# Performance work log

Measured on AMD Instinct MI355X. Metric: run time of the kernel, lower is better.

## Reference

```python
import jax, jax.numpy as jnp
import numpy as np

LN_EPS = 1e-5
CLAMP = 1e-8


def _linear(x, W, b):
    return x @ W + b


def _layernorm(x, g, b):
    mu = x.mean(-1, keepdims=True)
    var = ((x - mu) ** 2).mean(-1, keepdims=True)
    return (x - mu) / jnp.sqrt(var + LN_EPS) * g + b


def _residual(x, W1, b1, W2, b2):
    return jax.nn.relu(_linear(jax.nn.relu(_linear(x, W1, b1)), W2, b2)) + x


def _forward(node_emb, attn_Wq, attn_bq, attn_Wk, attn_bk, attn_Wv, attn_bv,
             attn_Wd, attn_bd, attn_ln_g, attn_ln_b,
             mlp_r1_w1, mlp_r1_b1, mlp_r1_w2, mlp_r1_b2,
             mlp_r2_w1, mlp_r2_b1, mlp_r2_w2, mlp_r2_b2,
             mlp_out_w, mlp_out_b,
             log_phi_r0, log_phi_r1h, log_phi_r1v, log_phi_r2, r0_idx, n):
    x = node_emb  # [1, n^2, D]
    L = attn_Wq.shape[0]
    for l in range(L):  # mask in the original is all zeros -> plain softmax attention
        q = _linear(x, attn_Wq[l], attn_bq[l])
        k = _linear(x, attn_Wk[l], attn_bk[l])
        v = _linear(x, attn_Wv[l], attn_bv[l])
        probs = jax.nn.softmax(jnp.einsum('bqd,bkd->bqk', q, k), axis=-1)
        ctx = jnp.einsum('bqk,bkd->bqd', probs, v)
        x = _layernorm(_linear(ctx, attn_Wd[l], attn_bd[l]) + x, attn_ln_g[l], attn_ln_b[l])
    x0 = x[0]                                  # [n^2, D]
    feats = x0[r0_idx].reshape(r0_idx.shape[0], -1)  # [R0, 4D]
    h = _residual(feats, mlp_r1_w1, mlp_r1_b1, mlp_r1_w2, mlp_r1_b2)
    h = _residual(h, mlp_r2_w1, mlp_r2_b1, mlp_r2_w2, mlp_r2_b2)
    logits = _linear(h, mlp_out_w, mlp_out_b)  # [R0, 16]
    beliefs = jax.nn.softmax(logits, axis=-1).reshape(-1, 2, 2, 2, 2)

    m = n - 1  # plaquettes per row
    # --- R1 horizontal interior edges (row r in 1..n-2, col c in 0..n-2) ---
    r, c = np.meshgrid(np.arange(1, n - 1), np.arange(m), indexing='ij')
    above = ((r - 1) * m + c).ravel()
    below = (r * m + c).ravel()
    h_stack = jnp.stack([beliefs[above].sum((1, 2)),   # edge nodes at plaquette pos 2,3
                         beliefs[below].sum((3, 4))])  # edge nodes at plaquette pos 0,1
    h_bel = h_stack.mean(0)                            # [Eh,2,2]
    mism = jnp.sum((h_stack - h_bel) ** 2)
    # --- R1 vertical interior edges (row r in 0..n-2, col c in 1..n-2) ---
    r, c = np.meshgrid(np.arange(m), np.arange(1, n - 1), indexing='ij')
    left = (r * m + (c - 1)).ravel()
    right = (r * m + c).ravel()
    v_stack = jnp.stack([beliefs[left].sum((1, 3)),    # edge nodes at pos 1,3
                         beliefs[right].sum((2, 4))])  # edge nodes at pos 0,2
    v_bel = v_stack.mean(0)                            # [Ev,2,2]
    mism = mism + jnp.sum((v_stack - v_bel) ** 2)
    # --- R2 interior nodes (r, c in 1..n-2), parents are the 4 incident edges ---
    r, c = np.meshgrid(np.arange(1, n - 1), np.arange(1, n - 1), indexing='ij')
    hl = ((r - 1) * m + (c - 1)).ravel()
    hr = ((r - 1) * m + c).ravel()
    vu = ((r - 1) * (n - 2) + (c - 1)).ravel()
    vd = (r * (n - 2) + (c - 1)).ravel()
    n_stack = jnp.stack([h_bel[hl].sum(1), h_bel[hr].sum(2),
                         v_bel[vu].sum(1), v_bel[vd].sum(2)])
    n_bel = n_stack.mean(0)                            # [V,2]
    mism = mism + jnp.sum((n_stack - n_bel) ** 2)

    # --- Kikuchi energy: counts +1 (plaquette), -1 (edge), +1 (node); log_phi detached ---
    def reg_energy(b, lphi, cnt):
        bc = jnp.maximum(b, CLAMP)
        return cnt * jnp.sum(bc * (jnp.log(bc) - jax.lax.stop_gradient(lphi)))

    energy = (reg_energy(beliefs, log_phi_r0, 1.0)
              + reg_energy(h_bel, log_phi_r1h, -1.0)
              + reg_energy(v_bel, log_phi_r1v, -1.0)
              + reg_energy(n_bel, log_phi_r2, 1.0))
    return energy, mism


def setup_inputs() -> dict:
    n, D, L, HID, OUT = 64, 256, 2, 1024, 16
    m = n - 1
    R0, E, V = m * m, (n - 2) * m, (n - 2) * (n - 2)
    key = jax.random.key(0)
    ks = jax.random.split(key, 24)
    norm = lambda k, sh, s=0.05: jax.random.normal(k, sh, dtype=jnp.float32) * s
    r, c = np.meshgrid(np.arange(m), np.arange(m), indexing='ij')
    i = (r * n + c).ravel()
    r0_idx = jnp.asarray(np.stack([i, i + 1, i + n, i + n + 1], 1), dtype=jnp.int32)
    inp = {
        'node_emb': jax.random.normal(ks[0], (1, n * n, D), dtype=jnp.float32),
        'attn_Wq': norm(ks[1], (L, D, D)), 'attn_bq': jnp.zeros((L, D), jnp.float32),
        'attn_Wk': norm(ks[2], (L, D, D)), 'attn_bk': jnp.zeros((L, D), jnp.float32),
        'attn_Wv': norm(ks[3], (L, D, D)), 'attn_bv': jnp.zeros((L, D), jnp.float32),
        'attn_Wd': norm(ks[4], (L, D, D)), 'attn_bd': jnp.zeros((L, D), jnp.float32),
        'attn_ln_g': jnp.ones((L, D), jnp.float32), 'attn_ln_b': jnp.zeros((L, D), jnp.float32),
        'mlp_r1_w1': norm(ks[5], (HID, HID), 0.03), 'mlp_r1_b1': jnp.zeros((HID,), jnp.float32),
        'mlp_r1_w2': norm(ks[6], (HID, HID), 0.03), 'mlp_r1_b2': jnp.zeros((HID,), jnp.float32),
        'mlp_r2_w1': norm(ks[7], (HID, HID), 0.03), 'mlp_r2_b1': jnp.zeros((HID,), jnp.float32),
        'mlp_r2_w2': norm(ks[8], (HID, HID), 0.03), 'mlp_r2_b2': jnp.zeros((HID,), jnp.float32),
        'mlp_out_w': norm(ks[9], (HID, OUT), 0.03), 'mlp_out_b': jnp.zeros((OUT,), jnp.float32),
        'log_phi_r0': jax.random.normal(ks[10], (R0, 2, 2, 2, 2), dtype=jnp.float32),
        'log_phi_r1h': jax.random.normal(ks[11], (E, 2, 2), dtype=jnp.float32),
        'log_phi_r1v': jax.random.normal(ks[12], (E, 2, 2), dtype=jnp.float32),
        'log_phi_r2': jax.random.normal(ks[13], (V, 2), dtype=jnp.float32),
        'r0_idx': r0_idx,
        'n': n,
    }
    return inp


def reference(node_emb, attn_Wq, attn_bq, attn_Wk, attn_bk, attn_Wv, attn_bv,
              attn_Wd, attn_bd, attn_ln_g, attn_ln_b,
              mlp_r1_w1, mlp_r1_b1, mlp_r1_w2, mlp_r1_b2,
              mlp_r2_w1, mlp_r2_b1, mlp_r2_w2, mlp_r2_b2,
              mlp_out_w, mlp_out_b,
              log_phi_r0, log_phi_r1h, log_phi_r1v, log_phi_r2, r0_idx, n):
    return _forward(node_emb, attn_Wq, attn_bq, attn_Wk, attn_bk, attn_Wv, attn_bv,
                    attn_Wd, attn_bd, attn_ln_g, attn_ln_b,
                    mlp_r1_w1, mlp_r1_b1, mlp_r1_w2, mlp_r1_b2,
                    mlp_r2_w1, mlp_r2_b1, mlp_r2_w2, mlp_r2_b2,
                    mlp_out_w, mlp_out_b,
                    log_phi_r0, log_phi_r1h, log_phi_r1v, log_phi_r2, r0_idx, n)
```

## Files before the change

kernel.cpp:

```cpp
#include <hip/hip_runtime.h>
#include <hip/hip_bf16.h>
#include <math.h>

#define D_    256
#define NSQ   4096
#define NL    2
#define HID_  1024
#define R0_   3969
#define EH_   3906
#define EV_   3906
#define NV_   3844
#define LN_EPS_ 1e-5f
#define CLAMP_  1e-8f
#define TK_    64

typedef float f32x4 __attribute__((ext_vector_type(4)));
typedef __bf16 bf16x8 __attribute__((ext_vector_type(8)));
typedef unsigned short u16x8 __attribute__((ext_vector_type(8)));

__device__ __forceinline__ void gload_lds16(const void* g, void* l) {
    __builtin_amdgcn_global_load_lds(
        (const __attribute__((address_space(1))) void*)g,
        (__attribute__((address_space(3))) void*)l, 16, 0, 0);
}

template<int BM, int BN>
__device__ __forceinline__ void gemm_body(
    const __hip_bfloat16* __restrict__ A, const __hip_bfloat16* __restrict__ Bt,
    const float* __restrict__ bias,
    const float* __restrict__ resf, const __hip_bfloat16* __restrict__ resb,
    void* __restrict__ C, int M, int N, int K, int relu, int outmode,
    int bx, int by)
{
    constexpr int WR  = BM / 64;
    constexpr int WC  = 4 / WR;
    constexpr int WNT = BN / WC;
    constexpr int NF  = WNT / 16;
    constexpr int ACH = BM / 64;
    constexpr int BCH = BN / 64;
    constexpr int ASZ = BM * 32;

    __shared__ __hip_bfloat16 sm[2][(BM + BN) * 32];

    const int t = threadIdx.x;
    const int lane = t & 63, wave = t >> 6;
    const int ln = lane & 15, lg = lane >> 4;
    const int wr = (WR == 1) ? 0 : (wave >> 1);
    const int wc = (WR == 1) ? wave : (wave & 1);
    const int row0 = bx * BM, col0 = by * BN;

    int aoff[ACH], boff[BCH];
    #pragma unroll
    for (int c = 0; c < ACH; ++c) {
        int e = (c * 256 + t) * 8;
        int row = e >> 5, slot = (e >> 3) & 3;
        int kg = slot ^ (row & 3) ^ ((row >> 2) & 3);
        aoff[c] = row * K + kg * 8;
    }
    #pragma unroll
    for (int c = 0; c < BCH; ++c) {
        int e = (c * 256 + t) * 8;
        int row = e >> 5, slot = (e >> 3) & 3;
        int kg = slot ^ (row & 3) ^ ((row >> 2) & 3);
        boff[c] = row * K + kg * 8;
    }
    const int sw = (ln & 3) ^ ((ln >> 2) & 3);

    const __hip_bfloat16* Ab = A + (size_t)row0 * K;
    const __hip_bfloat16* Bb = Bt + (size_t)col0 * K;

    f32x4 acc[4][NF];
    #pragma unroll
    for (int m = 0; m < 4; ++m)
        #pragma unroll
        for (int n = 0; n < NF; ++n) acc[m][n] = f32x4{0.f, 0.f, 0.f, 0.f};

    auto STAGE = [&](int k0, int buf) {
        #pragma unroll
        for (int c = 0; c < ACH; ++c)
            gload_lds16(Ab + k0 + aoff[c], (char*)&sm[buf][0] + (c * 256 + t) * 16);
        #pragma unroll
        for (int c = 0; c < BCH; ++c)
            gload_lds16(Bb + k0 + boff[c], (char*)&sm[buf][ASZ] + (c * 256 + t) * 16);
    };

    STAGE(0, 0);
    __syncthreads();
    int cur = 0;
    for (int k0 = 0; k0 < K; k0 += 32) {
        if (k0 + 32 < K) STAGE(k0 + 32, cur ^ 1);
        bf16x8 af[4], bfr[NF];
        #pragma unroll
        for (int m = 0; m < 4; ++m)
            af[m] = *(const bf16x8*)((const char*)&sm[cur][0] +
                     (size_t)(wr * 64 + m * 16 + ln) * 64 + ((lg ^ sw) << 4));
        #pragma unroll
        for (int n = 0; n < NF; ++n)
            bfr[n] = *(const bf16x8*)((const char*)&sm[cur][ASZ] +
                     (size_t)(wc * WNT + n * 16 + ln) * 64 + ((lg ^ sw) << 4));
        #pragma unroll
        for (int m = 0; m < 4; ++m)
            #pragma unroll
            for (int n = 0; n < NF; ++n)
                acc[m][n] = __builtin_amdgcn_mfma_f32_16x16x32_bf16(
                    af[m], bfr[n], acc[m][n], 0, 0, 0);
        __syncthreads();
        cur ^= 1;
    }

    #pragma unroll
    for (int m = 0; m < 4; ++m) {
        const int rowb = row0 + wr * 64 + m * 16 + lg * 4;
        #pragma unroll
        for (int n = 0; n < NF; ++n) {
            const int col = col0 + wc * WNT + n * 16 + ln;
            const float bv = bias ? bias[col] : 0.f;
            if (outmode == 2) {
                union { ushort4 u4; __hip_bfloat16 h[4]; } pk;
                #pragma unroll
                for (int r = 0; r < 4; ++r) {
                    float v = acc[m][n][r] + bv;
                    if (relu) v = fmaxf(v, 0.f);
                    pk.h[r] = __float2bfloat16(v);
                }
                *(ushort4*)((__hip_bfloat16*)C + (size_t)col * M + rowb) = pk.u4;
            } else if (outmode == 3) {
                union { ushort4 u4; __hip_bfloat16 h[4]; } pk;
                #pragma unroll
                for (int r = 0; r < 4; ++r) {
                    float v = acc[m][n][r] + bv;
                    if (relu) v = fmaxf(v, 0.f);
                    pk.h[r] = __float2bfloat16(v);
                }
                size_t off = ((size_t)((rowb >> 5) * 16 + (col >> 4)) << 9)
                           + (size_t)(((rowb >> 3) & 3) * 16 + (col & 15)) * 8
                           + (rowb & 7);
                *(ushort4*)((__hip_bfloat16*)C + off) = pk.u4;
            } else {
                #pragma unroll
                for (int r = 0; r < 4; ++r) {
                    float v = acc[m][n][r] + bv;
                    if (relu) v = fmaxf(v, 0.f);
                    const size_t idx = (size_t)(rowb + r) * N + col;
                    if (resf) v += resf[idx];
                    if (resb) v += __bfloat162float(resb[idx]);
                    if (outmode == 0) ((float*)C)[idx] = v;
                    else ((__hip_bfloat16*)C)[idx] = __float2bfloat16(v);
                }
            }
        }
    }
}

template<int BM, int BN>
__global__ __launch_bounds__(256) void gemm_t(
    const __hip_bfloat16* __restrict__ A, const __hip_bfloat16* __restrict__ Bt,
    const float* __restrict__ bias,
    const float* __restrict__ resf, const __hip_bfloat16* __restrict__ resb,
    void* __restrict__ C, int M, int N, int K, int relu, int outmode)
{
    gemm_body<BM, BN>(A, Bt, bias, resf, resb, C, M, N, K, relu, outmode,
                      blockIdx.x, blockIdx.y);
}

__global__ __launch_bounds__(256) void gemm_qkv(
    const __hip_bfloat16* __restrict__ xb,
    const __hip_bfloat16* __restrict__ wqkt2, const __hip_bfloat16* __restrict__ wvt2,
    const float* __restrict__ bqk2, const float* __restrict__ bv,
    __hip_bfloat16* __restrict__ qkb, __hip_bfloat16* __restrict__ vf, int l)
{
    const __hip_bfloat16* Bt;
    const float* bias;
    void* C;
    int N, outmode, by;
    if (blockIdx.y < 4) {
        Bt = wqkt2 + (size_t)l * 131072; bias = bqk2 + l * 512;
        C = qkb; N = 512; outmode = 1; by = blockIdx.y;
    } else {
        Bt = wvt2 + (size_t)l * 65536; bias = bv + l * D_;
        C = vf; N = D_; outmode = 3; by = blockIdx.y - 4;
    }
    gemm_body<64, 128>(xb, Bt, bias, nullptr, nullptr, C, NSQ, N, D_, 0, outmode,
                       blockIdx.x, by);
}

__global__ __launch_bounds__(512, 4) void gemm_128(
    const __hip_bfloat16* __restrict__ A, const __hip_bfloat16* __restrict__ Bt,
    const float* __restrict__ bias, const __hip_bfloat16* __restrict__ resb,
    __hip_bfloat16* __restrict__ C, int M, int N, int K, int relu)
{
    __shared__ __hip_bfloat16 sm[2][8192];

    const int t = threadIdx.x;
    const int lane = t & 63, wave = t >> 6;
    const int ln = lane & 15, lg = lane >> 4;
    const int wr = wave >> 2, wc = wave & 3;
    const int row0 = blockIdx.x * 128, col0 = blockIdx.y * 128;

    const int srow = t >> 2, sslot = t & 3;
    const int skg = sslot ^ (srow & 3) ^ ((srow >> 2) & 3);
    const int soff = srow * K + skg * 8;
    const int sw = (ln & 3) ^ ((ln >> 2) & 3);

    const __hip_bfloat16* Ab = A + (size_t)row0 * K;
    const __hip_bfloat16* Bb = Bt + (size_t)col0 * K;

    f32x4 acc[4][2];
    #pragma unroll
    for (int m = 0; m < 4; ++m)
        #pragma unroll
        for (int n = 0; n < 2; ++n) acc[m][n] = f32x4{0.f, 0.f, 0.f, 0.f};

    auto STAGE = [&](int k0, int buf) {
        gload_lds16(Ab + k0 + soff, (char*)&sm[buf][0] + t * 16);
        gload_lds16(Bb + k0 + soff, (char*)&sm[buf][4096] + t * 16);
    };

    STAGE(0, 0);
    __syncthreads();
    int cur = 0;
    for (int k0 = 0; k0 < K; k0 += 32) {
        if (k0 + 32 < K) STAGE(k0 + 32, cur ^ 1);
        bf16x8 af[4], bfr[2];
        #pragma unroll
        for (int m = 0; m < 4; ++m)
            af[m] = *(const bf16x8*)((const char*)&sm[cur][0] +
                     (size_t)(wr * 64 + m * 16 + ln) * 64 + ((lg ^ sw) << 4));
        #pragma unroll
        for (int n = 0; n < 2; ++n)
            bfr[n] = *(const bf16x8*)((const char*)&sm[cur][4096] +
                     (size_t)(wc * 32 + n * 16 + ln) * 64 + ((lg ^ sw) << 4));
        #pragma unroll
        for (int m = 0; m < 4; ++m)
            #pragma unroll
            for (int n = 0; n < 2; ++n)
                acc[m][n] = __builtin_amdgcn_mfma_f32_16x16x32_bf16(
                    af[m], bfr[n], acc[m][n], 0, 0, 0);
        __syncthreads();
        cur ^= 1;
    }

    #pragma unroll
    for (int m = 0; m < 4; ++m) {
        const int rowb = row0 + wr * 64 + m * 16 + lg * 4;
        #pragma unroll
        for (int n = 0; n < 2; ++n) {
            const int col = col0 + wc * 32 + n * 16 + ln;
            const float bv = bias[col];
            #pragma unroll
            for (int r = 0; r < 4; ++r) {
                float v = acc[m][n][r] + bv;
                if (relu) v = fmaxf(v, 0.f);
                const size_t idx = (size_t)(rowb + r) * N + col;
                if (resb) v += __bfloat162float(resb[idx]);
                C[idx] = __float2bfloat16(v);
            }
        }
    }
}

__global__ __launch_bounds__(256) void gemm_n16b(
    const __hip_bfloat16* __restrict__ A, const __hip_bfloat16* __restrict__ Bt,
    const float* __restrict__ bias, const float* __restrict__ lphi0,
    float* __restrict__ beliefs, float* __restrict__ out, int M, int K)
{
    const int t = threadIdx.x, lane = t & 63, wave = t >> 6;
    const int ln = lane & 15, lg = lane >> 4;
    const int r0 = blockIdx.x * 64 + wave * 16;
    f32x4 acc = {0.f, 0.f, 0.f, 0.f};
    for (int k0 = 0; k0 < K; k0 += 32) {
        bf16x8 a = *(const bf16x8*)(A + (size_t)(r0 + ln) * K + k0 + lg * 8);
        bf16x8 b = *(const bf16x8*)(Bt + (size_t)ln * K + k0 + lg * 8);
        acc = __builtin_amdgcn_mfma_f32_16x16x32_bf16(a, b, acc, 0, 0, 0);
    }
    float e = 0.f;
    #pragma unroll
    for (int r = 0; r < 4; ++r) {
        const int row = r0 + lg * 4 + r;
        float v = acc[r] + bias[ln];
        float mx = v;
        mx = fmaxf(mx, __shfl_xor(mx, 1));
        mx = fmaxf(mx, __shfl_xor(mx, 2));
        mx = fmaxf(mx, __shfl_xor(mx, 4));
        mx = fmaxf(mx, __shfl_xor(mx, 8));
        float ex = __expf(v - mx);
        float s = ex;
        s += __shfl_xor(s, 1);
        s += __shfl_xor(s, 2);
        s += __shfl_xor(s, 4);
        s += __shfl_xor(s, 8);
        if (row < R0_) {
            float bb = ex / s;
            beliefs[(size_t)row * 16 + ln] = bb;
            float bc = fmaxf(bb, CLAMP_);
            e += bc * (logf(bc) - lphi0[(size_t)row * 16 + ln]);
        }
    }
    #pragma unroll
    for (int off = 32; off; off >>= 1) e += __shfl_down(e, off);
    if (lane == 0) atomicAdd(&out[0], e);
}

__global__ __launch_bounds__(256) void prep_k(
    const float* __restrict__ node_emb, __hip_bfloat16* __restrict__ xb,
    const float* __restrict__ outw, __hip_bfloat16* __restrict__ outwt,
    const float* __restrict__ Wq, const float* __restrict__ Wk,
    const float* __restrict__ Wv, const float* __restrict__ Wd,
    __hip_bfloat16* __restrict__ wqkt2, __hip_bfloat16* __restrict__ wvt2,
    __hip_bfloat16* __restrict__ wdt2,
    const float* __restrict__ bq, const float* __restrict__ bk,
    float* __restrict__ bqk2,
    const float* __restrict__ M0, const float* __restrict__ M1,
    const float* __restrict__ M2, const float* __restrict__ M3,
    __hip_bfloat16* __restrict__ T0, __hip_bfloat16* __restrict__ T1,
    __hip_bfloat16* __restrict__ T2, __hip_bfloat16* __restrict__ T3)
{
    __shared__ float tile[32][33];
    const int b = blockIdx.x, t = threadIdx.x;
    if (b < 1024) {
        int p = b * 256 + t;
        float4 v = *(const float4*)(node_emb + (size_t)p * 4);
        union { ushort4 u4; __hip_bfloat16 h[4]; } pk;
        pk.h[0] = __float2bfloat16(v.x); pk.h[1] = __float2bfloat16(v.y);
        pk.h[2] = __float2bfloat16(v.z); pk.h[3] = __float2bfloat16(v.w);
        *(ushort4*)(xb + (size_t)p * 4) = pk.u4;
    } else if (b < 1088) {
        int i = (b - 1024) * 256 + t;
        int n = i >> 10, k = i & 1023;
        outwt[i] = __float2bfloat16(outw[k * 16 + n]);
    } else if (b < 1600) {
        int idx = b - 1088;
        int z = idx >> 6, bx = (idx >> 3) & 7, by = idx & 7;
        int l = z >> 2, w = z & 3;
        const float* W = (w == 0 ? Wq : w == 1 ? Wk : w == 2 ? Wv : Wd) + (size_t)l * 65536;
        __hip_bfloat16* Wt = w == 0 ? wqkt2 + (size_t)l * 131072
                           : w == 1 ? wqkt2 + (size_t)l * 131072 + 65536
                           : w == 2 ? wvt2 + (size_t)l * 65536
                                    : wdt2 + (size_t)l * 65536;
        int k0 = bx * 32, n0 = by * 32;
        int r = t >> 3, c4 = (t & 7) * 4;
        float4 v = *(const float4*)(W + (size_t)(k0 + r) * 256 + n0 + c4);
        tile[r][c4 + 0] = v.x; tile[r][c4 + 1] = v.y;
        tile[r][c4 + 2] = v.z; tile[r][c4 + 3] = v.w;
        __syncthreads();
        union { ushort4 u4; __hip_bfloat16 h[4]; } pk;
        #pragma unroll
        for (int i = 0; i < 4; ++i) pk.h[i] = __float2bfloat16(tile[c4 + i][r]);
        *(ushort4*)(Wt + (size_t)(n0 + r) * 256 + k0 + c4) = pk.u4;
    } else if (b < 1604) {
        int idx = (b - 1600) * 256 + t;
        int l = idx >> 9, j = idx & 511;
        bqk2[idx] = j < 256 ? bq[l * 256 + j] : bk[l * 256 + j - 256];
    } else {
        int idx = b - 1604;
        int z = idx >> 10, rem = idx & 1023;
        const float* W = z == 0 ? M0 : z == 1 ? M1 : z == 2 ? M2 : M3;
        __hip_bfloat16* Wt = z == 0 ? T0 : z == 1 ? T1 : z == 2 ? T2 : T3;
        int k0 = (rem >> 5) * 32, n0 = (rem & 31) * 32;
        int r = t >> 3, c4 = (t & 7) * 4;
        float4 v = *(const float4*)(W + (size_t)(k0 + r) * 1024 + n0 + c4);
        tile[r][c4 + 0] = v.x; tile[r][c4 + 1] = v.y;
        tile[r][c4 + 2] = v.z; tile[r][c4 + 3] = v.w;
        __syncthreads();
        union { ushort4 u4; __hip_bfloat16 h[4]; } pk;
        #pragma unroll
        for (int i = 0; i < 4; ++i) pk.h[i] = __float2bfloat16(tile[c4 + i][r]);
        *(ushort4*)(Wt + (size_t)(n0 + r) * 1024 + k0 + c4) = pk.u4;
    }
}

template<int KS>
__global__ __launch_bounds__(512, 2) void attn_mfma_t(
    const __hip_bfloat16* __restrict__ qk, const __hip_bfloat16* __restrict__ vf,
    __hip_bfloat16* __restrict__ po, float* __restrict__ pm, float* __restrict__ pl)
{
    constexpr int KRANGE = NSQ / KS;
    constexpr int NT = KRANGE / TK_;
    constexpr int VOFF = 65536;
    constexpr int POFF = 98304;
    const int t = threadIdx.x;
    const int wave = t >> 6, lane = t & 63;
    const int ln = lane & 15, lg = lane >> 4;
    const int q0 = blockIdx.x * 128 + wave * 16;
    const int ks = blockIdx.y;
    const int k0 = ks * KRANGE;

    __shared__ __align__(16) char smem[116736];

    bf16x8 qa[8];
    #pragma unroll
    for (int s = 0; s < 8; ++s)
        qa[s] = *(const bf16x8*)(qk + (size_t)(q0 + ln) * 512 + s * 32 + lg * 8);

    int srcoff[4];
    #pragma unroll
    for (int c = 0; c < 4; ++c) {
        int row = c * 16 + (t >> 5);
        int g = (t & 31) ^ ((row & 15) << 1);
        srcoff[c] = row * 512 + 256 + g * 8;
    }
    int rb[8];
    #pragma unroll
    for (int s8 = 0; s8 < 8; ++s8)
        rb[s8] = ln * 512 + (((s8 * 4 + lg) ^ (ln << 1)) << 4);

    f32x4 o[16];
    #pragma unroll
    for (int nt = 0; nt < 16; ++nt) o[nt] = f32x4{0.f, 0.f, 0.f, 0.f};
    float rm = -1e30f, rl = 0.f;

    {
        const __hip_bfloat16* src = qk + (size_t)k0 * 512;
        #pragma unroll
        for (int c = 0; c < 4; ++c)
            gload_lds16(src + srcoff[c], smem + c * 8192 + t * 16);
    }
    __syncthreads();

    for (int it = 0; it < NT; ++it) {
        const int cur = it & 1;
        {
            const __hip_bfloat16* vsrc = vf + ((size_t)((k0 + it * TK_) >> 5) << 13);
            #pragma unroll
            for (int c = 0; c < 4; ++c) {
                int idx = c * 512 + t;
                gload_lds16(vsrc + (size_t)idx * 8, smem + VOFF + idx * 16);
            }
        }
        {
            const int itn = (it + 1 < NT) ? it + 1 : it;
            const __hip_bfloat16* src = qk + (size_t)(k0 + itn * TK_) * 512;
            #pragma unroll
            for (int c = 0; c < 4; ++c)
                gload_lds16(src + srcoff[c], smem + (cur ^ 1) * 32768 + c * 8192 + t * 16);
        }
        const char* kbase = smem + cur * 32768;
        f32x4 s4[4];
        #pragma unroll
        for (int nt = 0; nt < 4; ++nt) {
            f32x4 acc = {0.f, 0.f, 0.f, 0.f};
            #pragma unroll
            for (int s8 = 0; s8 < 8; ++s8) {
                bf16x8 kb = *(const bf16x8*)(kbase + nt * 8192 + rb[s8]);
                acc = __builtin_amdgcn_mfma_f32_16x16x32_bf16(kb, qa[s8], acc, 0, 0, 0);
            }
            s4[nt] = acc;
        }
        float mx = -1e30f;
        #pragma unroll
        for (int nt = 0; nt < 4; ++nt)
            #pragma unroll
            for (int r = 0; r < 4; ++r) mx = fmaxf(mx, s4[nt][r]);
        mx = fmaxf(mx, __shfl_xor(mx, 16));
        mx = fmaxf(mx, __shfl_xor(mx, 32));
        float sc = 1.f;
        if (__any(mx > rm + 8.f)) {
            float mnew = fmaxf(rm, mx);
            sc = __expf(rm - mnew);
            rm = mnew;
            float scr[4];
            #pragma unroll
            for (int r = 0; r < 4; ++r) scr[r] = __shfl(sc, lg * 4 + r);
            #pragma unroll
            for (int nt = 0; nt < 16; ++nt)
                #pragma unroll
                for (int r = 0; r < 4; ++r) o[nt][r] *= scr[r];
        }
        float rs = 0.f;
        #pragma unroll
        for (int nt = 0; nt < 4; ++nt)
            #pragma unroll
            for (int r = 0; r < 4; ++r) {
                float p = __expf(s4[nt][r] - rm);
                s4[nt][r] = p;
                rs += p;
            }
        rs += __shfl_xor(rs, 16);
        rs += __shfl_xor(rs, 32);
        rl = rl * sc + rs;
        char* prow = smem + POFF + wave * 2304 + ln * 144;
        #pragma unroll
        for (int nt = 0; nt < 4; ++nt) {
            union { ushort4 u4; __hip_bfloat16 h[4]; } pk;
            #pragma unroll
            for (int r = 0; r < 4; ++r) pk.h[r] = __float2bfloat16(s4[nt][r]);
            *(ushort4*)(prow + nt * 32 + lg * 8) = pk.u4;
        }
        asm volatile("s_waitcnt lgkmcnt(0)" ::: "memory");
        __builtin_amdgcn_sched_barrier(0);
        bf16x8 pa0 = *(const bf16x8*)(prow + lg * 16);
        bf16x8 pa1 = *(const bf16x8*)(prow + 64 + lg * 16);
        asm volatile("s_waitcnt vmcnt(4)" ::: "memory");
        __builtin_amdgcn_sched_barrier(0);
        __builtin_amdgcn_s_barrier();
        const char* vl = smem + VOFF;
        #pragma unroll
        for (int ntd = 0; ntd < 16; ++ntd) {
            bf16x8 vb0 = *(const bf16x8*)(vl + ntd * 1024 + lane * 16);
            bf16x8 vb1 = *(const bf16x8*)(vl + 16384 + ntd * 1024 + lane * 16);
            o[ntd] = __builtin_amdgcn_mfma_f32_16x16x32_bf16(pa0, vb0, o[ntd], 0, 0, 0);
            o[ntd] = __builtin_amdgcn_mfma_f32_16x16x32_bf16(pa1, vb1, o[ntd], 0, 0, 0);
        }
        __syncthreads();
    }
    unsigned short* ob = (unsigned short*)(smem + wave * 8448);
    #pragma unroll
    for (int nt = 0; nt < 16; ++nt)
        #pragma unroll
        for (int r = 0; r < 4; ++r) {
            __hip_bfloat16 h = __float2bfloat16(o[nt][r]);
            ob[(lg * 4 + r) * 264 + nt * 16 + ln] = *(unsigned short*)&h;
        }
    asm volatile("s_waitcnt lgkmcnt(0)" ::: "memory");
    __builtin_amdgcn_sched_barrier(0);
    unsigned short* pob = (unsigned short*)po;
    #pragma unroll
    for (int i = 0; i < 8; ++i) {
        int f = i * 64 + lane;
        int row = f >> 5, dc = f & 31;
        u16x8 vv = *(const u16x8*)(ob + row * 264 + dc * 8);
        *(u16x8*)(pob + ((size_t)ks * NSQ + q0 + row) * D_ + dc * 8) = vv;
    }
    if (lane < 16) {
        pm[ks * NSQ + q0 + lane] = rm;
        pl[ks * NSQ + q0 + lane] = rl;
    }
}

template<int KS>
__global__ __launch_bounds__(256) void attn_combine_t(
    const __hip_bfloat16* __restrict__ po, const float* __restrict__ pm,
    const float* __restrict__ pl, __hip_bfloat16* __restrict__ ctx)
{
    const int idx8 = blockIdx.x * 256 + threadIdx.x;
    const int row = idx8 >> 5;
    float m[KS], ms = -1e30f;
    #pragma unroll
    for (int s = 0; s < KS; ++s) { m[s] = pm[s * NSQ + row]; ms = fmaxf(ms, m[s]); }
    float l = 0.f, w[KS];
    #pragma unroll
    for (int s = 0; s < KS; ++s) {
        w[s] = __expf(m[s] - ms);
        l += w[s] * pl[s * NSQ + row];
    }
    const float inv = 1.f / l;
    float num[8];
    #pragma unroll
    for (int j = 0; j < 8; ++j) num[j] = 0.f;
    #pragma unroll
    for (int s = 0; s < KS; ++s) {
        u16x8 v = *(const u16x8*)(po + (size_t)s * (NSQ * D_) + (size_t)idx8 * 8);
        #pragma unroll
        for (int j = 0; j < 8; ++j) {
            union { float f; unsigned u; } cv;
            cv.u = (unsigned)v[j] << 16;
            num[j] += w[s] * cv.f;
        }
    }
    union { u16x8 u8; __hip_bfloat16 h[8]; } pk;
    #pragma unroll
    for (int j = 0; j < 8; ++j) pk.h[j] = __float2bfloat16(num[j] * inv);
    *(u16x8*)(ctx + (size_t)idx8 * 8) = pk.u8;
}

__global__ __launch_bounds__(256) void ln_f32(
    const float* __restrict__ y, const float* __restrict__ g,
    const float* __restrict__ b, float* __restrict__ xo,
    __hip_bfloat16* __restrict__ xob, __hip_bfloat16* __restrict__ feats, int fin)
{
    const int lane = threadIdx.x & 63, wave = threadIdx.x >> 6;
    const int row = blockIdx.x * 4 + wave;
    float4 v = *(const float4*)(y + (size_t)row * D_ + lane * 4);
    float s = v.x + v.y + v.z + v.w;
    #pragma unroll
    for (int off = 1; off < 64; off <<= 1) s += __shfl_xor(s, off);
    float mu = s * (1.f / D_);
    float dx = v.x - mu, dy = v.y - mu, dz = v.z - mu, dw = v.w - mu;
    float q = dx * dx + dy * dy + dz * dz + dw * dw;
    #pragma unroll
    for (int off = 1; off < 64; off <<= 1) q += __shfl_xor(q, off);
    float inv = rsqrtf(q * (1.f / D_) + LN_EPS_);
    float4 gg = *(const float4*)(g + lane * 4);
    float4 bb = *(const float4*)(b + lane * 4);
    float4 o;
    o.x = dx * inv * gg.x + bb.x;
    o.y = dy * inv * gg.y + bb.y;
    o.z = dz * inv * gg.z + bb.z;
    o.w = dw * inv * gg.w + bb.w;
    union { ushort4 u4; __hip_bfloat16 h[4]; } pk;
    pk.h[0] = __float2bfloat16(o.x); pk.h[1] = __float2bfloat16(o.y);
    pk.h[2] = __float2bfloat16(o.z); pk.h[3] = __float2bfloat16(o.w);
    if (!fin) {
        *(float4*)(xo + (size_t)row * D_ + lane * 4) = o;
        *(ushort4*)(xob + (size_t)row * D_ + lane * 4) = pk.u4;
    } else {
        const int r = row >> 6, c = row & 63;
        if (r < 63 && c < 63)
            *(ushort4*)(feats + (size_t)(r * 63 + c) * 1024 + lane * 4) = pk.u4;
        if (r < 63 && c > 0)
            *(ushort4*)(feats + (size_t)(r * 63 + c - 1) * 1024 + 256 + lane * 4) = pk.u4;
        if (r > 0 && c < 63)
            *(ushort4*)(feats + (size_t)((r - 1) * 63 + c) * 1024 + 512 + lane * 4) = pk.u4;
        if (r > 0 && c > 0)
            *(ushort4*)(feats + (size_t)((r - 1) * 63 + c - 1) * 1024 + 768 + lane * 4) = pk.u4;
    }
}

__global__ __launch_bounds__(256) void edges_k(
    const float* __restrict__ beliefs, const float* __restrict__ lphih,
    const float* __restrict__ lphiv, float* __restrict__ hbel,
    float* __restrict__ vbel, float* __restrict__ out)
{
    int e = blockIdx.x * 256 + threadIdx.x;
    float el = 0.f, ml = 0.f;
    if (blockIdx.y == 0) {
        if (e < EH_) {
            const float* bA = beliefs + (size_t)e * 16;
            const float* bB = beliefs + (size_t)(e + 63) * 16;
            float s0[4] = {0,0,0,0}, s1[4] = {0,0,0,0};
            #pragma unroll
            for (int ab = 0; ab < 4; ++ab)
                #pragma unroll
                for (int cd = 0; cd < 4; ++cd) {
                    s0[cd] += bA[ab * 4 + cd];
                    s1[ab] += bB[ab * 4 + cd];
                }
            #pragma unroll
            for (int z = 0; z < 4; ++z) {
                float hb = 0.5f * (s0[z] + s1[z]);
                hbel[e * 4 + z] = hb;
                float d0 = s0[z] - hb, d1 = s1[z] - hb;
                ml += d0 * d0 + d1 * d1;
                float bc = fmaxf(hb, CLAMP_);
                el -= bc * (logf(bc) - lphih[e * 4 + z]);
            }
        }
    } else {
        if (e < EV_) {
            int r = e / 62, c = e % 62 + 1;
            const float* bL = beliefs + (size_t)(r * 63 + c - 1) * 16;
            const float* bR = beliefs + (size_t)(r * 63 + c) * 16;
            float s0[4] = {0,0,0,0}, s1[4] = {0,0,0,0};
            #pragma unroll
            for (int a = 0; a < 2; ++a)
                #pragma unroll
                for (int bq = 0; bq < 2; ++bq)
                    #pragma unroll
                    for (int c2 = 0; c2 < 2; ++c2)
                        #pragma unroll
                        for (int d = 0; d < 2; ++d) {
                            int idx = a * 8 + bq * 4 + c2 * 2 + d;
                            s0[bq * 2 + d]  += bL[idx];
                            s1[a * 2 + c2] += bR[idx];
                        }
            #pragma unroll
            for (int z = 0; z < 4; ++z) {
                float vb = 0.5f * (s0[z] + s1[z]);
                vbel[e * 4 + z] = vb;
                float d0 = s0[z] - vb, d1 = s1[z] - vb;
                ml += d0 * d0 + d1 * d1;
                float bc = fmaxf(vb, CLAMP_);
                el -= bc * (logf(bc) - lphiv[e * 4 + z]);
            }
        }
    }
    for (int off = 32; off; off >>= 1) { el += __shfl_down(el, off); ml += __shfl_down(ml, off); }
    if ((threadIdx.x & 63) == 0) { atomicAdd(&out[0], el); atomicAdd(&out[1], ml); }
}

__global__ __launch_bounds__(256) void node_k(
    const float* __restrict__ hbel, const float* __restrict__ vbel,
    const float* __restrict__ lphi2, float* __restrict__ out)
{
    int vtx = blockIdx.x * 256 + threadIdx.x;
    float el = 0.f, ml = 0.f;
    if (vtx < NV_) {
        int hl = (vtx / 62) * 63 + (vtx % 62);
        int hr = hl + 1;
        int vu = vtx;
        int vd = vtx + 62;
        float n0[2], n1[2], n2[2], n3[2];
        #pragma unroll
        for (int z = 0; z < 2; ++z) {
            n0[z] = hbel[hl * 4 + z] + hbel[hl * 4 + 2 + z];
            n1[z] = hbel[hr * 4 + z * 2] + hbel[hr * 4 + z * 2 + 1];
            n2[z] = vbel[vu * 4 + z] + vbel[vu * 4 + 2 + z];
            n3[z] = vbel[vd * 4 + z * 2] + vbel[vd * 4 + z * 2 + 1];
        }
        #pragma unroll
        for (int z = 0; z < 2; ++z) {
            float nb = 0.25f * (n0[z] + n1[z] + n2[z] + n3[z]);
            float d0 = n0[z] - nb, d1 = n1[z] - nb, d2 = n2[z] - nb, d3 = n3[z] - nb;
            ml += d0 * d0 + d1 * d1 + d2 * d2 + d3 * d3;
            float bc = fmaxf(nb, CLAMP_);
            el += bc * (logf(bc) - lphi2[vtx * 2 + z]);
        }
    }
    for (int off = 32; off; off >>= 1) { el += __shfl_down(el, off); ml += __shfl_down(ml, off); }
    if ((threadIdx.x & 63) == 0) { atomicAdd(&out[0], el); atomicAdd(&out[1], ml); }
}

extern "C" void kernel_launch(void* const* d_in, const int* in_sizes, int n_in,
                              void* d_out, int out_size, void* d_ws, size_t ws_size,
                              hipStream_t stream)
{
    (void)in_sizes; (void)n_in; (void)out_size; (void)ws_size;
    const float* node_emb = (const float*)d_in[0];
    const float* Wq  = (const float*)d_in[1];
    const float* bq  = (const float*)d_in[2];
    const float* Wk  = (const float*)d_in[3];
    const float* bk  = (const float*)d_in[4];
    const float* Wv  = (const float*)d_in[5];
    const float* bv  = (const float*)d_in[6];
    const float* Wd  = (const float*)d_in[7];
    const float* bd  = (const float*)d_in[8];
    const float* lng = (const float*)d_in[9];
    const float* lnb = (const float*)d_in[10];
    const float* r1w1 = (const float*)d_in[11];
    const float* r1b1 = (const float*)d_in[12];
    const float* r1w2 = (const float*)d_in[13];
    const float* r1b2 = (const float*)d_in[14];
    const float* r2w1 = (const float*)d_in[15];
    const float* r2b1 = (const float*)d_in[16];
    const float* r2w2 = (const float*)d_in[17];
    const float* r2b2 = (const float*)d_in[18];
    const float* outw = (const float*)d_in[19];
    const float* outb = (const float*)d_in[20];
    const float* lphi0 = (const float*)d_in[21];
    const float* lphih = (const float*)d_in[22];
    const float* lphiv = (const float*)d_in[23];
    const float* lphi2 = (const float*)d_in[24];

    float* ws = (float*)d_ws;
    float* x      = ws;
    __hip_bfloat16* xb = (__hip_bfloat16*)(ws + 1048576);
    float* belief = ws + 1638400;
    float* hbel   = ws + 1703936;
    float* vbel   = ws + 1720320;
    __hip_bfloat16* outwt = (__hip_bfloat16*)(ws + 1736704);
    float* arena  = ws + 1744896;

    __hip_bfloat16* wqkt2 = (__hip_bfloat16*)(arena);
    __hip_bfloat16* wvt2  = (__hip_bfloat16*)(arena + 131072);
    __hip_bfloat16* wdt2  = (__hip_bfloat16*)(arena + 196608);
    float* bqk2 = arena + 262144;
    __hip_bfloat16* qkb = (__hip_bfloat16*)(arena + 263168);
    __hip_bfloat16* vf  = (__hip_bfloat16*)(arena + 1311744);
    __hip_bfloat16* ctxb = vf;
    float* yb = arena + 1836032;
    float* pm = arena + 2884608;
    float* pl = arena + 2950144;
    __hip_bfloat16* po = (__hip_bfloat16*)(arena + 3015680);

    __hip_bfloat16* feats = (__hip_bfloat16*)(ws + 8954880);
    __hip_bfloat16* w1t = (__hip_bfloat16*)(ws + 11052032);
    __hip_bfloat16* w2t = (__hip_bfloat16*)(ws + 11576320);
    __hip_bfloat16* w3t = (__hip_bfloat16*)(ws + 12100608);
    __hip_bfloat16* w4t = (__hip_bfloat16*)(ws + 12624896);
    __hip_bfloat16* hA  = (__hip_bfloat16*)(arena);
    __hip_bfloat16* hB  = (__hip_bfloat16*)(arena + 2097152);

    hipMemsetAsync(d_out, 0, 2 * sizeof(float), stream);

    dim3 blk(256);
    dim3 blk512(512);
    prep_k<<<dim3(5700), blk, 0, stream>>>(node_emb, xb, outw, outwt,
                                           Wq, Wk, Wv, Wd, wqkt2, wvt2, wdt2,
                                           bq, bk, bqk2,
                                           r1w1, r1w2, r2w1, r2w2,
                                           w1t, w2t, w3t, w4t);

    for (int l = 0; l < NL; ++l) {
        gemm_qkv<<<dim3(64, 6), blk, 0, stream>>>(xb, wqkt2, wvt2, bqk2, bv,
                                                  qkb, vf, l);
        attn_mfma_t<8><<<dim3(NSQ / 128, 8), blk512, 0, stream>>>(qkb, vf, po, pm, pl);
        attn_combine_t<8><<<dim3(NSQ * D_ / 2048), blk, 0, stream>>>(po, pm, pl, ctxb);
        gemm_t<64, 64><<<dim3(NSQ / 64, D_ / 64), blk, 0, stream>>>(
            ctxb, wdt2 + (size_t)l * 65536, bd + l * D_,
            (l == 0 ? node_emb : x), nullptr, yb, NSQ, D_, D_, 0, 0);
        ln_f32<<<dim3(NSQ / 4), blk, 0, stream>>>(yb, lng + l * D_, lnb + l * D_,
                                                  x, xb, feats, l);
    }

    dim3 gM(NSQ / 128, HID_ / 128);
    gemm_128<<<gM, blk512, 0, stream>>>(feats, w1t, r1b1, nullptr,
                                        hA, NSQ, HID_, HID_, 1);
    gemm_128<<<gM, blk512, 0, stream>>>(hA, w2t, r1b2, feats,
                                        hB, NSQ, HID_, HID_, 1);
    gemm_128<<<gM, blk512, 0, stream>>>(hB, w3t, r2b1, nullptr,
                                        hA, NSQ, HID_, HID_, 1);
    gemm_128<<<gM, blk512, 0, stream>>>(hA, w4t, r2b2, hB,
                                        feats, NSQ, HID_, HID_, 1);

    float* outp = (float*)d_out;
    gemm_n16b<<<dim3(NSQ / 64), blk, 0, stream>>>(feats, outwt, outb, lphi0,
                                                  belief, outp, NSQ, HID_);
    edges_k<<<dim3((EH_ + 255) / 256, 2), blk, 0, stream>>>(belief, lphih, lphiv,
                                                            hbel, vbel, outp);
    node_k<<<dim3((NV_ + 255) / 256), blk, 0, stream>>>(hbel, vbel, lphi2, outp);
}
```

Measured before the change: 238.1 us.

## Pipeline MLP GEMM with 4-stage LDS ring and fold output memset into prep

After: 230.8 us. -3.0%, faster.

```diff
diff --git a/kernel.cpp b/kernel.cpp
--- a/kernel.cpp
+++ b/kernel.cpp
@@ -184,68 +184,82 @@
                        blockIdx.x, by);
 }
 
-__global__ __launch_bounds__(512, 4) void gemm_128(
+__global__ __launch_bounds__(256, 2) void gemm_128p(
     const __hip_bfloat16* __restrict__ A, const __hip_bfloat16* __restrict__ Bt,
     const float* __restrict__ bias, const __hip_bfloat16* __restrict__ resb,
     __hip_bfloat16* __restrict__ C, int M, int N, int K, int relu)
 {
-    __shared__ __hip_bfloat16 sm[2][8192];
+    __shared__ __hip_bfloat16 sm[4][8192];
 
     const int t = threadIdx.x;
     const int lane = t & 63, wave = t >> 6;
     const int ln = lane & 15, lg = lane >> 4;
-    const int wr = wave >> 2, wc = wave & 3;
+    const int wr = wave >> 1, wc = wave & 1;
     const int row0 = blockIdx.x * 128, col0 = blockIdx.y * 128;
 
-    const int srow = t >> 2, sslot = t & 3;
-    const int skg = sslot ^ (srow & 3) ^ ((srow >> 2) & 3);
-    const int soff = srow * K + skg * 8;
+    int aoff[2];
+    #pragma unroll
+    for (int c = 0; c < 2; ++c) {
+        int e = (c * 256 + t) * 8;
+        int row = e >> 5, slot = (e >> 3) & 3;
+        int kg = slot ^ (row & 3) ^ ((row >> 2) & 3);
+        aoff[c] = row * K + kg * 8;
+    }
     const int sw = (ln & 3) ^ ((ln >> 2) & 3);
 
     const __hip_bfloat16* Ab = A + (size_t)row0 * K;
     const __hip_bfloat16* Bb = Bt + (size_t)col0 * K;
 
-    f32x4 acc[4][2];
+    f32x4 acc[4][4];
     #pragma unroll
     for (int m = 0; m < 4; ++m)
         #pragma unroll
-        for (int n = 0; n < 2; ++n) acc[m][n] = f32x4{0.f, 0.f, 0.f, 0.f};
+        for (int n = 0; n < 4; ++n) acc[m][n] = f32x4{0.f, 0.f, 0.f, 0.f};
 
     auto STAGE = [&](int k0, int buf) {
-        gload_lds16(Ab + k0 + soff, (char*)&sm[buf][0] + t * 16);
-        gload_lds16(Bb + k0 + soff, (char*)&sm[buf][4096] + t * 16);
+        #pragma unroll
+        for (int c = 0; c < 2; ++c) {
+            gload_lds16(Ab + k0 + aoff[c], (char*)&sm[buf][0] + (c * 256 + t) * 16);
+            gload_lds16(Bb + k0 + aoff[c], (char*)&sm[buf][4096] + (c * 256 + t) * 16);
+        }
     };
 
-    STAGE(0, 0);
-    __syncthreads();
-    int cur = 0;
-    for (int k0 = 0; k0 < K; k0 += 32) {
-        if (k0 + 32 < K) STAGE(k0 + 32, cur ^ 1);
-        bf16x8 af[4], bfr[2];
+    const int NT = K >> 5;
+    STAGE(0, 0); STAGE(32, 1); STAGE(64, 2);
+
+    for (int tt = 0; tt < NT; ++tt) {
+        const int rem = NT - 1 - tt;
+        if (rem >= 2)      asm volatile("s_waitcnt vmcnt(8)" ::: "memory");
+        else if (rem == 1) asm volatile("s_waitcnt vmcnt(4)" ::: "memory");
+        else               asm volatile("s_waitcnt vmcnt(0)" ::: "memory");
+        __builtin_amdgcn_sched_barrier(0);
+        __builtin_amdgcn_s_barrier();
+        if (tt + 3 < NT) STAGE((tt + 3) * 32, (tt + 3) & 3);
+
+        const char* base = (const char*)&sm[tt & 3][0];
+        bf16x8 af[4], bfr[4];
         #pragma unroll
         for (int m = 0; m < 4; ++m)
-            af[m] = *(const bf16x8*)((const char*)&sm[cur][0] +
+            af[m] = *(const bf16x8*)(base +
                      (size_t)(wr * 64 + m * 16 + ln) * 64 + ((lg ^ sw) << 4));
         #pragma unroll
-        for (int n = 0; n < 2; ++n)
-            bfr[n] = *(const bf16x8*)((const char*)&sm[cur][4096] +
-                     (size_t)(wc * 32 + n * 16 + ln) * 64 + ((lg ^ sw) << 4));
+        for (int n = 0; n < 4; ++n)
+            bfr[n] = *(const bf16x8*)(base + 8192 +
+                     (size_t)(wc * 64 + n * 16 + ln) * 64 + ((lg ^ sw) << 4));
         #pragma unroll
         for (int m = 0; m < 4; ++m)
             #pragma unroll
-            for (int n = 0; n < 2; ++n)
+            for (int n = 0; n < 4; ++n)
                 acc[m][n] = __builtin_amdgcn_mfma_f32_16x16x32_bf16(
                     af[m], bfr[n], acc[m][n], 0, 0, 0);
-        __syncthreads();
-        cur ^= 1;
     }
 
     #pragma unroll
     for (int m = 0; m < 4; ++m) {
         const int rowb = row0 + wr * 64 + m * 16 + lg * 4;
         #pragma unroll
-        for (int n = 0; n < 2; ++n) {
-            const int col = col0 + wc * 32 + n * 16 + ln;
+        for (int n = 0; n < 4; ++n) {
+            const int col = col0 + wc * 64 + n * 16 + ln;
             const float bv = bias[col];
             #pragma unroll
             for (int r = 0; r < 4; ++r) {
@@ -313,10 +327,12 @@
     const float* __restrict__ M0, const float* __restrict__ M1,
     const float* __restrict__ M2, const float* __restrict__ M3,
     __hip_bfloat16* __restrict__ T0, __hip_bfloat16* __restrict__ T1,
-    __hip_bfloat16* __restrict__ T2, __hip_bfloat16* __restrict__ T3)
+    __hip_bfloat16* __restrict__ T2, __hip_bfloat16* __restrict__ T3,
+    float* __restrict__ outp)
 {
     __shared__ float tile[32][33];
     const int b = blockIdx.x, t = threadIdx.x;
+    if (b == 0 && t < 2) outp[t] = 0.f;
     if (b < 1024) {
         int p = b * 256 + t;
         float4 v = *(const float4*)(node_emb + (size_t)p * 4);
@@ -760,15 +776,14 @@
     __hip_bfloat16* hA  = (__hip_bfloat16*)(arena);
     __hip_bfloat16* hB  = (__hip_bfloat16*)(arena + 2097152);
 
-    hipMemsetAsync(d_out, 0, 2 * sizeof(float), stream);
-
+    float* outp = (float*)d_out;
     dim3 blk(256);
     dim3 blk512(512);
     prep_k<<<dim3(5700), blk, 0, stream>>>(node_emb, xb, outw, outwt,
                                            Wq, Wk, Wv, Wd, wqkt2, wvt2, wdt2,
                                            bq, bk, bqk2,
                                            r1w1, r1w2, r2w1, r2w2,
-                                           w1t, w2t, w3t, w4t);
+                                           w1t, w2t, w3t, w4t, outp);
 
     for (int l = 0; l < NL; ++l) {
         gemm_qkv<<<dim3(64, 6), blk, 0, stream>>>(xb, wqkt2, wvt2, bqk2, bv,
@@ -783,16 +798,15 @@
     }
 
     dim3 gM(NSQ / 128, HID_ / 128);
-    gemm_128<<<gM, blk512, 0, stream>>>(feats, w1t, r1b1, nullptr,
-                                        hA, NSQ, HID_, HID_, 1);
-    gemm_128<<<gM, blk512, 0, stream>>>(hA, w2t, r1b2, feats,
-                                        hB, NSQ, HID_, HID_, 1);
-    gemm_128<<<gM, blk512, 0, stream>>>(hB, w3t, r2b1, nullptr,
-                                        hA, NSQ, HID_, HID_, 1);
-    gemm_128<<<gM, blk512, 0, stream>>>(hA, w4t, r2b2, hB,
-                                        feats, NSQ, HID_, HID_, 1);
-
-    float* outp = (float*)d_out;
+    gemm_128p<<<gM, blk, 0, stream>>>(feats, w1t, r1b1, nullptr,
+                                      hA, NSQ, HID_, HID_, 1);
+    gemm_128p<<<gM, blk, 0, stream>>>(hA, w2t, r1b2, feats,
+                                      hB, NSQ, HID_, HID_, 1);
+    gemm_128p<<<gM, blk, 0, stream>>>(hB, w3t, r2b1, nullptr,
+                                      hA, NSQ, HID_, HID_, 1);
+    gemm_128p<<<gM, blk, 0, stream>>>(hA, w4t, r2b2, hB,
+                                      feats, NSQ, HID_, HID_, 1);
+
     gemm_n16b<<<dim3(NSQ / 64), blk, 0, stream>>>(feats, outwt, outb, lphi0,
                                                   belief, outp, NSQ, HID_);
     edges_k<<<dim3((EH_ + 255) / 256, 2), blk, 0, stream>>>(belief, lphih, lphiv,
```
